# Kernel optimization log

Measured on AMD Instinct MI355X. Metric: run time of the kernel, lower is better.

Reference implementation:

```python
import jax, jax.numpy as jnp
import numpy as np


def setup_inputs() -> dict:
    key = jax.random.key(0)
    k1, k2, k3, k4 = jax.random.split(key, 4)
    B, T, C, H = 4, 2048, 1024, 64
    x = jax.random.normal(k1, (B, T, C), dtype=jnp.float32)
    # nn.Linear(n_embd, head_size, bias=False) weights, stored as [in, out]
    s = 1.0 / np.sqrt(C)
    Wk = jax.random.normal(k2, (C, H), dtype=jnp.float32) * s
    Wq = jax.random.normal(k3, (C, H), dtype=jnp.float32) * s
    Wv = jax.random.normal(k4, (C, H), dtype=jnp.float32) * s
    return {"x": x, "Wk": Wk, "Wq": Wq, "Wv": Wv}


def reference(x, Wk, Wq, Wv):
    B, T, C = x.shape
    k = x @ Wk  # [B,T,H]
    q = x @ Wq  # [B,T,H]
    v = x @ Wv  # [B,T,H]
    # NOTE: original scales by C**-0.5 where C = n_embd (faithful quirk).
    scale = jnp.asarray(C, x.dtype) ** -0.5
    wei = jnp.einsum('bth,bsh->bts', q, k) * scale  # [B,T,T]
    causal = jnp.tril(jnp.ones((T, T), dtype=bool))
    wei = jnp.where(causal, wei, -jnp.inf)
    wei = jax.nn.softmax(wei, axis=-1)
    # dropout is identity in eval mode / for deterministic reference
    return jnp.einsum('bts,bsh->bth', wei, v)
```

## Files before the change

kernel.cpp:

```cpp
#include <hip/hip_runtime.h>

#define B_ 4
#define T_ 2048
#define C_ 1024
#define H_ 64
#define M_ (B_*T_)

typedef __bf16 bf16x8 __attribute__((ext_vector_type(8)));
typedef float f32x4 __attribute__((ext_vector_type(4)));
typedef short short8 __attribute__((ext_vector_type(8)));
typedef short short4v __attribute__((ext_vector_type(4)));
typedef float float4v __attribute__((ext_vector_type(4)));

static __device__ __forceinline__ f32x4 mfma16(bf16x8 a, bf16x8 b, f32x4 c) {
    return __builtin_amdgcn_mfma_f32_16x16x32_bf16(a, b, c, 0, 0, 0);
}
static __device__ __forceinline__ unsigned short f2bfu(float f) {
    return __builtin_bit_cast(unsigned short, (__bf16)f);
}

__global__ __launch_bounds__(256) void wconv_kernel(const float* __restrict__ Wk,
                                                    const float* __restrict__ Wq,
                                                    const float* __restrict__ Wv,
                                                    unsigned short* __restrict__ Wtf) {
    int t = blockIdx.x * 256 + threadIdx.x;
    int f = t >> 6;
    int l = t & 63;
    int n = f % 12, kk = f / 12;
    int sel = n >> 2;
    int wcol = (n & 3) * 16 + (l & 15);
    int kbase = kk * 32 + (l >> 4) * 8;
    const float* W = (sel == 0) ? Wk : ((sel == 1) ? Wq : Wv);
    float scale = (sel == 1) ? 0.03125f : 1.0f;
    unsigned short* dst = Wtf + f * 512 + l * 8;
#pragma unroll
    for (int j = 0; j < 8; ++j)
        dst[j] = f2bfu(W[(kbase + j) * 64 + wcol] * scale);
}

__global__ __launch_bounds__(256) void proj_kernel(const float* __restrict__ x,
                                                   const unsigned short* __restrict__ Wtf,
                                                   unsigned short* __restrict__ kbuf,
                                                   unsigned short* __restrict__ qbuf,
                                                   unsigned short* __restrict__ vbuf) {
    int tid = threadIdx.x;
    int l = tid & 63, lm = l & 15, lg = l >> 4;
    int w = tid >> 6;
    int r0 = blockIdx.x * 16;

    f32x4 acc[3];
#pragma unroll
    for (int nn = 0; nn < 3; ++nn) acc[nn] = f32x4{0.f, 0.f, 0.f, 0.f};

    const float* xp = x + (r0 + lm) * C_ + lg * 8;
    const unsigned short* wp = Wtf + (w * 3) * 512 + l * 8;

    float4v a0 = *(const float4v*)(xp);
    float4v a1 = *(const float4v*)(xp + 4);
    short8 b0 = *(const short8*)(wp);
    short8 b1 = *(const short8*)(wp + 512);
    short8 b2 = *(const short8*)(wp + 1024);

    for (int kk = 0; kk < 31; ++kk) {
        xp += 32; wp += 12 * 512;
        float4v na0 = *(const float4v*)(xp);
        float4v na1 = *(const float4v*)(xp + 4);
        short8 nb0 = *(const short8*)(wp);
        short8 nb1 = *(const short8*)(wp + 512);
        short8 nb2 = *(const short8*)(wp + 1024);
        bf16x8 af;
#pragma unroll
        for (int j = 0; j < 4; ++j) { af[j] = (__bf16)a0[j]; af[4 + j] = (__bf16)a1[j]; }
        acc[0] = mfma16(af, __builtin_bit_cast(bf16x8, b0), acc[0]);
        acc[1] = mfma16(af, __builtin_bit_cast(bf16x8, b1), acc[1]);
        acc[2] = mfma16(af, __builtin_bit_cast(bf16x8, b2), acc[2]);
        a0 = na0; a1 = na1; b0 = nb0; b1 = nb1; b2 = nb2;
    }
    {
        bf16x8 af;
#pragma unroll
        for (int j = 0; j < 4; ++j) { af[j] = (__bf16)a0[j]; af[4 + j] = (__bf16)a1[j]; }
        acc[0] = mfma16(af, __builtin_bit_cast(bf16x8, b0), acc[0]);
        acc[1] = mfma16(af, __builtin_bit_cast(bf16x8, b1), acc[1]);
        acc[2] = mfma16(af, __builtin_bit_cast(bf16x8, b2), acc[2]);
    }

    int tg0 = r0 + lg * 4;
#pragma unroll
    for (int nn = 0; nn < 3; ++nn) {
        int n = w * 3 + nn;
        int sel = n >> 2;
        int col = (n & 3) * 16 + lm;
        unsigned short* dst = (sel == 0) ? kbuf : ((sel == 1) ? qbuf : vbuf);
#pragma unroll
        for (int i = 0; i < 4; ++i)
            dst[(tg0 + i) * H_ + col] = f2bfu(acc[nn][i]);
    }
}

__global__ __launch_bounds__(256) void kvconv_kernel(unsigned short* __restrict__ kbuf,
                                                     unsigned short* __restrict__ vbuf) {
    __shared__ alignas(16) unsigned short klds[32][72];
    __shared__ alignas(16) unsigned short vlds[32][72];
    int tid = threadIdx.x;
    int bj = blockIdx.x;
    unsigned short* kt = kbuf + bj * 2048;
    unsigned short* vt = vbuf + bj * 2048;

    int row = tid >> 3, cq = (tid & 7) * 8;
    short8 kv = *(const short8*)(kt + row * 64 + cq);
    short8 vv = *(const short8*)(vt + row * 64 + cq);
    *(short8*)(&klds[row][cq]) = kv;
    *(short8*)(&vlds[row][cq]) = vv;
    __syncthreads();

    int l = tid & 63, lm = l & 15, lg = l >> 4;
    int f = tid >> 6;
    int kk = f >> 1, nn = f & 1;
    short8 kf = *(const short8*)(&klds[nn * 16 + lm][kk * 32 + lg * 8]);
    short8 vf;
#pragma unroll
    for (int jj = 0; jj < 8; ++jj)
        vf[jj] = (short)vlds[lg * 8 + jj][f * 16 + lm];

    *(short8*)(kt + f * 512 + l * 8) = kf;
    *(short8*)(vt + f * 512 + l * 8) = vf;
}

__global__ __launch_bounds__(512) void attn_kernel(const unsigned short* __restrict__ kbuf,
                                                   const unsigned short* __restrict__ qbuf,
                                                   const unsigned short* __restrict__ vbuf,
                                                   float* __restrict__ out) {
    int tid = threadIdx.x;
    int l = tid & 63, lm = l & 15, lg = l >> 4;
    int w = tid >> 6;
    int bid = blockIdx.x;
    int xcd = bid & 7, ii = bid >> 3;
    int b = xcd >> 1;
    int qtl = ii * 2 + (xcd & 1);
    int q0 = (127 - qtl) * 16;

    __shared__ alignas(16) unsigned short plds[8][16][72];
    __shared__ float olds[8][16][64];
    __shared__ float mlds[8][16];
    __shared__ float llds[8][16];

    bf16x8 qf[2];
#pragma unroll
    for (int kk = 0; kk < 2; ++kk)
        qf[kk] = __builtin_bit_cast(bf16x8,
            *(const short8*)(qbuf + (b * T_ + q0 + lm) * H_ + kk * 32 + lg * 8));

    f32x4 of[4];
#pragma unroll
    for (int nh = 0; nh < 4; ++nh) of[nh] = f32x4{0.f, 0.f, 0.f, 0.f};
    float mrun = -1e30f, lrun = 0.f;

    int nj = q0 / 64 + 1;

    for (int J = w; J < nj; J += 8) {
        f32x4 s[4];
#pragma unroll
        for (int n = 0; n < 4; ++n) s[n] = f32x4{0.f, 0.f, 0.f, 0.f};
#pragma unroll
        for (int kk = 0; kk < 2; ++kk) {
#pragma unroll
            for (int n = 0; n < 4; ++n) {
                const unsigned short* kp = kbuf +
                    (((b * 64 + 2 * J + (n >> 1)) * 2 + kk) * 2 + (n & 1)) * 512 + l * 8;
                s[n] = mfma16(__builtin_bit_cast(bf16x8, *(const short8*)kp), qf[kk], s[n]);
            }
        }
        if (J == nj - 1) {
            int qr = q0 + lm;
#pragma unroll
            for (int n = 0; n < 4; ++n) {
                int kc0 = J * 64 + (n >> 1) * 32 + (n & 1) * 16 + lg * 4;
#pragma unroll
                for (int i = 0; i < 4; ++i)
                    if (kc0 + i > qr) s[n][i] = -1e30f;
            }
        }
        float pm0 = fmaxf(fmaxf(s[0][0], s[0][1]), fmaxf(s[0][2], s[0][3]));
        float pm1 = fmaxf(fmaxf(s[1][0], s[1][1]), fmaxf(s[1][2], s[1][3]));
        float pm2 = fmaxf(fmaxf(s[2][0], s[2][1]), fmaxf(s[2][2], s[2][3]));
        float pm3 = fmaxf(fmaxf(s[3][0], s[3][1]), fmaxf(s[3][2], s[3][3]));
        float pm = fmaxf(fmaxf(pm0, pm1), fmaxf(pm2, pm3));
        pm = fmaxf(pm, __shfl_xor(pm, 16, 64));
        pm = fmaxf(pm, __shfl_xor(pm, 32, 64));
        float mn = fmaxf(mrun, pm);
        float al = __expf(mrun - mn);
        float rsn[4];
#pragma unroll
        for (int n = 0; n < 4; ++n) {
            float e0 = __expf(s[n][0] - mn), e1 = __expf(s[n][1] - mn);
            float e2 = __expf(s[n][2] - mn), e3 = __expf(s[n][3] - mn);
            s[n][0] = e0; s[n][1] = e1; s[n][2] = e2; s[n][3] = e3;
            rsn[n] = (e0 + e1) + (e2 + e3);
        }
        float rs = (rsn[0] + rsn[1]) + (rsn[2] + rsn[3]);
        rs += __shfl_xor(rs, 16, 64);
        rs += __shfl_xor(rs, 32, 64);
        lrun = lrun * al + rs;
        mrun = mn;
        float alv[4];
#pragma unroll
        for (int i = 0; i < 4; ++i) alv[i] = __shfl(al, lg * 4 + i, 64);
#pragma unroll
        for (int nh = 0; nh < 4; ++nh)
#pragma unroll
            for (int i = 0; i < 4; ++i) of[nh][i] *= alv[i];

#pragma unroll
        for (int n = 0; n < 4; ++n) {
            short4v pv;
#pragma unroll
            for (int i = 0; i < 4; ++i) pv[i] = (short)f2bfu(s[n][i]);
            *(short4v*)(&plds[w][lm][(n >> 1) * 32 + (n & 1) * 16 + lg * 4]) = pv;
        }
        bf16x8 pf[2];
#pragma unroll
        for (int ks = 0; ks < 2; ++ks)
            pf[ks] = __builtin_bit_cast(bf16x8,
                *(const short8*)(&plds[w][lm][ks * 32 + lg * 8]));
#pragma unroll
        for (int nh = 0; nh < 4; ++nh) {
#pragma unroll
            for (int ks = 0; ks < 2; ++ks) {
                const unsigned short* vp = vbuf +
                    ((b * 64 + 2 * J + ks) * 4 + nh) * 512 + l * 8;
                of[nh] = mfma16(pf[ks], __builtin_bit_cast(bf16x8, *(const short8*)vp), of[nh]);
            }
        }
    }

#pragma unroll
    for (int nh = 0; nh < 4; ++nh)
#pragma unroll
        for (int i = 0; i < 4; ++i)
            olds[w][lg * 4 + i][nh * 16 + lm] = of[nh][i];
    if (l < 16) {
        mlds[w][l] = mrun;
        llds[w][l] = lrun;
    }
    __syncthreads();

    int row = tid >> 5;
    int c0 = tid & 31;
    float mw[8];
#pragma unroll
    for (int u = 0; u < 8; ++u) mw[u] = mlds[u][row];
    float M = fmaxf(fmaxf(fmaxf(mw[0], mw[1]), fmaxf(mw[2], mw[3])),
                    fmaxf(fmaxf(mw[4], mw[5]), fmaxf(mw[6], mw[7])));
    float ew[8];
    float L = 0.f;
#pragma unroll
    for (int u = 0; u < 8; ++u) { ew[u] = __expf(mw[u] - M); L += llds[u][row] * ew[u]; }
    float invL = 1.0f / L;
#pragma unroll
    for (int h = 0; h < 2; ++h) {
        int col = c0 + h * 32;
        float o = 0.f;
#pragma unroll
        for (int u = 0; u < 8; ++u) o += olds[u][row][col] * ew[u];
        out[(b * T_ + q0 + row) * H_ + col] = o * invL;
    }
}

extern "C" void kernel_launch(void* const* d_in, const int* in_sizes, int n_in,
                              void* d_out, int out_size, void* d_ws, size_t ws_size,
                              hipStream_t stream) {
    const float* x  = (const float*)d_in[0];
    const float* Wk = (const float*)d_in[1];
    const float* Wq = (const float*)d_in[2];
    const float* Wv = (const float*)d_in[3];
    float* out = (float*)d_out;

    unsigned short* ws   = (unsigned short*)d_ws;
    unsigned short* Wtf  = ws;
    unsigned short* kbuf = Wtf + 384 * 512;
    unsigned short* qbuf = kbuf + M_ * H_;
    unsigned short* vbuf = qbuf + M_ * H_;

    wconv_kernel<<<dim3(96), dim3(256), 0, stream>>>(Wk, Wq, Wv, Wtf);
    proj_kernel<<<dim3(M_ / 16), dim3(256), 0, stream>>>(x, Wtf, kbuf, qbuf, vbuf);
    kvconv_kernel<<<dim3(B_ * 64), dim3(256), 0, stream>>>(kbuf, vbuf);
    attn_kernel<<<dim3(B_ * (T_ / 16)), dim3(512), 0, stream>>>(kbuf, qbuf, vbuf, out);
}
```

Baseline: 106.9 us.

## Merge all stages into one cooperative persistent kernel with grid syncs

```diff
diff --git a/kernel.cpp b/kernel.cpp
--- a/kernel.cpp
+++ b/kernel.cpp
@@ -1,4 +1,5 @@
 #include <hip/hip_runtime.h>
+#include <hip/hip_cooperative_groups.h>
 
 #define B_ 4
 #define T_ 2048
@@ -19,251 +20,254 @@
     return __builtin_bit_cast(unsigned short, (__bf16)f);
 }
 
-__global__ __launch_bounds__(256) void wconv_kernel(const float* __restrict__ Wk,
-                                                    const float* __restrict__ Wq,
-                                                    const float* __restrict__ Wv,
-                                                    unsigned short* __restrict__ Wtf) {
-    int t = blockIdx.x * 256 + threadIdx.x;
-    int f = t >> 6;
-    int l = t & 63;
-    int n = f % 12, kk = f / 12;
-    int sel = n >> 2;
-    int wcol = (n & 3) * 16 + (l & 15);
-    int kbase = kk * 32 + (l >> 4) * 8;
-    const float* W = (sel == 0) ? Wk : ((sel == 1) ? Wq : Wv);
-    float scale = (sel == 1) ? 0.03125f : 1.0f;
-    unsigned short* dst = Wtf + f * 512 + l * 8;
-#pragma unroll
-    for (int j = 0; j < 8; ++j)
-        dst[j] = f2bfu(W[(kbase + j) * 64 + wcol] * scale);
-}
-
-__global__ __launch_bounds__(256) void proj_kernel(const float* __restrict__ x,
-                                                   const unsigned short* __restrict__ Wtf,
-                                                   unsigned short* __restrict__ kbuf,
-                                                   unsigned short* __restrict__ qbuf,
-                                                   unsigned short* __restrict__ vbuf) {
+struct SmemAttn {
+    unsigned short plds[8][16][72];
+    float olds[8][16][64];
+    float mlds[8][16];
+    float llds[8][16];
+};
+struct SmemProj {
+    float red[2][12][64][4];
+    unsigned short stage[3][16][72];
+};
+union alignas(16) Smem { SmemAttn a; SmemProj p; };
+
+__global__ __launch_bounds__(512, 4) void mega_kernel(
+        const float* __restrict__ x,
+        const float* __restrict__ Wk, const float* __restrict__ Wq,
+        const float* __restrict__ Wv,
+        unsigned short* __restrict__ ws, float* __restrict__ out, int mode) {
+    __shared__ Smem sm;
+    unsigned short* Wtf  = ws;
+    unsigned short* kbuf = ws + 196608;
+    unsigned short* qfb  = kbuf + 524288;
+    unsigned short* vbuf = qfb + 524288;
+
     int tid = threadIdx.x;
+    int bid = blockIdx.x;
     int l = tid & 63, lm = l & 15, lg = l >> 4;
     int w = tid >> 6;
-    int r0 = blockIdx.x * 16;
-
-    f32x4 acc[3];
-#pragma unroll
-    for (int nn = 0; nn < 3; ++nn) acc[nn] = f32x4{0.f, 0.f, 0.f, 0.f};
-
-    const float* xp = x + (r0 + lm) * C_ + lg * 8;
-    const unsigned short* wp = Wtf + (w * 3) * 512 + l * 8;
-
-    float4v a0 = *(const float4v*)(xp);
-    float4v a1 = *(const float4v*)(xp + 4);
-    short8 b0 = *(const short8*)(wp);
-    short8 b1 = *(const short8*)(wp + 512);
-    short8 b2 = *(const short8*)(wp + 1024);
-
-    for (int kk = 0; kk < 31; ++kk) {
-        xp += 32; wp += 12 * 512;
-        float4v na0 = *(const float4v*)(xp);
-        float4v na1 = *(const float4v*)(xp + 4);
-        short8 nb0 = *(const short8*)(wp);
-        short8 nb1 = *(const short8*)(wp + 512);
-        short8 nb2 = *(const short8*)(wp + 1024);
-        bf16x8 af;
-#pragma unroll
-        for (int j = 0; j < 4; ++j) { af[j] = (__bf16)a0[j]; af[4 + j] = (__bf16)a1[j]; }
-        acc[0] = mfma16(af, __builtin_bit_cast(bf16x8, b0), acc[0]);
-        acc[1] = mfma16(af, __builtin_bit_cast(bf16x8, b1), acc[1]);
-        acc[2] = mfma16(af, __builtin_bit_cast(bf16x8, b2), acc[2]);
-        a0 = na0; a1 = na1; b0 = nb0; b1 = nb1; b2 = nb2;
-    }
+
+    if ((mode == 3 || mode == 0) && bid < 48) {
+        int t = bid * 512 + tid;
+        int f = t >> 6, la = t & 63;
+        int n = f % 12, kk = f / 12;
+        int sel = n >> 2;
+        int wcol = (n & 3) * 16 + (la & 15);
+        int kbase = kk * 32 + (la >> 4) * 8;
+        const float* W = (sel == 0) ? Wk : ((sel == 1) ? Wq : Wv);
+        float scale = (sel == 1) ? 0.03125f : 1.0f;
+        unsigned short* dst = Wtf + f * 512 + la * 8;
+#pragma unroll
+        for (int j = 0; j < 8; ++j)
+            dst[j] = f2bfu(W[(kbase + j) * 64 + wcol] * scale);
+    }
+    if (mode == 3) cooperative_groups::this_grid().sync();
+
+    if (mode == 3 || mode == 1) {
+        int r0 = bid * 16;
+        int khalf = w >> 2;
+        int c3 = (w & 3) * 3;
+        f32x4 acc[3];
+#pragma unroll
+        for (int nn = 0; nn < 3; ++nn) acc[nn] = f32x4{0.f, 0.f, 0.f, 0.f};
+
+        const float* xp = x + (r0 + lm) * C_ + khalf * 512 + lg * 8;
+        const unsigned short* wp = Wtf + (khalf * 16 * 12 + c3) * 512 + l * 8;
+
+        float4v a0 = *(const float4v*)(xp);
+        float4v a1 = *(const float4v*)(xp + 4);
+        short8 b0 = *(const short8*)(wp);
+        short8 b1 = *(const short8*)(wp + 512);
+        short8 b2 = *(const short8*)(wp + 1024);
+        for (int kk = 0; kk < 15; ++kk) {
+            xp += 32; wp += 12 * 512;
+            float4v na0 = *(const float4v*)(xp);
+            float4v na1 = *(const float4v*)(xp + 4);
+            short8 nb0 = *(const short8*)(wp);
+            short8 nb1 = *(const short8*)(wp + 512);
+            short8 nb2 = *(const short8*)(wp + 1024);
+            bf16x8 af;
+#pragma unroll
+            for (int j = 0; j < 4; ++j) { af[j] = (__bf16)a0[j]; af[4 + j] = (__bf16)a1[j]; }
+            acc[0] = mfma16(af, __builtin_bit_cast(bf16x8, b0), acc[0]);
+            acc[1] = mfma16(af, __builtin_bit_cast(bf16x8, b1), acc[1]);
+            acc[2] = mfma16(af, __builtin_bit_cast(bf16x8, b2), acc[2]);
+            a0 = na0; a1 = na1; b0 = nb0; b1 = nb1; b2 = nb2;
+        }
+        {
+            bf16x8 af;
+#pragma unroll
+            for (int j = 0; j < 4; ++j) { af[j] = (__bf16)a0[j]; af[4 + j] = (__bf16)a1[j]; }
+            acc[0] = mfma16(af, __builtin_bit_cast(bf16x8, b0), acc[0]);
+            acc[1] = mfma16(af, __builtin_bit_cast(bf16x8, b1), acc[1]);
+            acc[2] = mfma16(af, __builtin_bit_cast(bf16x8, b2), acc[2]);
+        }
+#pragma unroll
+        for (int nn = 0; nn < 3; ++nn)
+            *(f32x4*)&sm.p.red[khalf][c3 + nn][l][0] = acc[nn];
+        __syncthreads();
+
+        for (int idx = tid; idx < 768; idx += 512) {
+            int tile = idx >> 6, l2 = idx & 63, lm2 = l2 & 15, lg2 = l2 >> 4;
+            f32x4 s0 = *(const f32x4*)&sm.p.red[0][tile][l2][0];
+            f32x4 s1 = *(const f32x4*)&sm.p.red[1][tile][l2][0];
+            int sel = tile >> 2, colb = (tile & 3) * 16 + lm2;
+#pragma unroll
+            for (int i = 0; i < 4; ++i)
+                sm.p.stage[sel][lg2 * 4 + i][colb] = f2bfu(s0[i] + s1[i]);
+        }
+        __syncthreads();
+
+        int bq = bid >> 7;
+        int jt = (bid & 127) >> 1;
+        int nn = bid & 1;
+        int base = (bq * 64 + jt) * 2048;
+        if (w < 2) {
+            short8 v = *(const short8*)&sm.p.stage[0][lm][w * 32 + lg * 8];
+            *(short8*)(kbuf + base + w * 1024 + nn * 512 + l * 8) = v;
+        } else if (w < 4) {
+            int kkq = w - 2;
+            short8 v = *(const short8*)&sm.p.stage[1][lm][kkq * 32 + lg * 8];
+            *(short8*)(qfb + bid * 1024 + kkq * 512 + l * 8) = v;
+        } else if (l < 32) {
+            int nh = w - 4;
+            short8 v;
+#pragma unroll
+            for (int j = 0; j < 8; ++j)
+                v[j] = (short)sm.p.stage[2][(l >> 4) * 8 + j][nh * 16 + (l & 15)];
+            *(short8*)(vbuf + base + nh * 512 + nn * 256 + l * 8) = v;
+        }
+    }
+    if (mode == 3) cooperative_groups::this_grid().sync();
+
+    if (!(mode == 3 || mode == 2)) return;
     {
-        bf16x8 af;
-#pragma unroll
-        for (int j = 0; j < 4; ++j) { af[j] = (__bf16)a0[j]; af[4 + j] = (__bf16)a1[j]; }
-        acc[0] = mfma16(af, __builtin_bit_cast(bf16x8, b0), acc[0]);
-        acc[1] = mfma16(af, __builtin_bit_cast(bf16x8, b1), acc[1]);
-        acc[2] = mfma16(af, __builtin_bit_cast(bf16x8, b2), acc[2]);
-    }
-
-    int tg0 = r0 + lg * 4;
-#pragma unroll
-    for (int nn = 0; nn < 3; ++nn) {
-        int n = w * 3 + nn;
-        int sel = n >> 2;
-        int col = (n & 3) * 16 + lm;
-        unsigned short* dst = (sel == 0) ? kbuf : ((sel == 1) ? qbuf : vbuf);
-#pragma unroll
-        for (int i = 0; i < 4; ++i)
-            dst[(tg0 + i) * H_ + col] = f2bfu(acc[nn][i]);
-    }
-}
-
-__global__ __launch_bounds__(256) void kvconv_kernel(unsigned short* __restrict__ kbuf,
-                                                     unsigned short* __restrict__ vbuf) {
-    __shared__ alignas(16) unsigned short klds[32][72];
-    __shared__ alignas(16) unsigned short vlds[32][72];
-    int tid = threadIdx.x;
-    int bj = blockIdx.x;
-    unsigned short* kt = kbuf + bj * 2048;
-    unsigned short* vt = vbuf + bj * 2048;
-
-    int row = tid >> 3, cq = (tid & 7) * 8;
-    short8 kv = *(const short8*)(kt + row * 64 + cq);
-    short8 vv = *(const short8*)(vt + row * 64 + cq);
-    *(short8*)(&klds[row][cq]) = kv;
-    *(short8*)(&vlds[row][cq]) = vv;
-    __syncthreads();
-
-    int l = tid & 63, lm = l & 15, lg = l >> 4;
-    int f = tid >> 6;
-    int kk = f >> 1, nn = f & 1;
-    short8 kf = *(const short8*)(&klds[nn * 16 + lm][kk * 32 + lg * 8]);
-    short8 vf;
-#pragma unroll
-    for (int jj = 0; jj < 8; ++jj)
-        vf[jj] = (short)vlds[lg * 8 + jj][f * 16 + lm];
-
-    *(short8*)(kt + f * 512 + l * 8) = kf;
-    *(short8*)(vt + f * 512 + l * 8) = vf;
-}
-
-__global__ __launch_bounds__(512) void attn_kernel(const unsigned short* __restrict__ kbuf,
-                                                   const unsigned short* __restrict__ qbuf,
-                                                   const unsigned short* __restrict__ vbuf,
-                                                   float* __restrict__ out) {
-    int tid = threadIdx.x;
-    int l = tid & 63, lm = l & 15, lg = l >> 4;
-    int w = tid >> 6;
-    int bid = blockIdx.x;
-    int xcd = bid & 7, ii = bid >> 3;
-    int b = xcd >> 1;
-    int qtl = ii * 2 + (xcd & 1);
-    int q0 = (127 - qtl) * 16;
-
-    __shared__ alignas(16) unsigned short plds[8][16][72];
-    __shared__ float olds[8][16][64];
-    __shared__ float mlds[8][16];
-    __shared__ float llds[8][16];
-
-    bf16x8 qf[2];
-#pragma unroll
-    for (int kk = 0; kk < 2; ++kk)
-        qf[kk] = __builtin_bit_cast(bf16x8,
-            *(const short8*)(qbuf + (b * T_ + q0 + lm) * H_ + kk * 32 + lg * 8));
-
-    f32x4 of[4];
-#pragma unroll
-    for (int nh = 0; nh < 4; ++nh) of[nh] = f32x4{0.f, 0.f, 0.f, 0.f};
-    float mrun = -1e30f, lrun = 0.f;
-
-    int nj = q0 / 64 + 1;
-
-    for (int J = w; J < nj; J += 8) {
-        f32x4 s[4];
-#pragma unroll
-        for (int n = 0; n < 4; ++n) s[n] = f32x4{0.f, 0.f, 0.f, 0.f};
-#pragma unroll
-        for (int kk = 0; kk < 2; ++kk) {
+        int xcd = bid & 7, ii = bid >> 3;
+        int b = xcd >> 1;
+        int qtl = ii * 2 + (xcd & 1);
+        int q0 = (127 - qtl) * 16;
+
+        bf16x8 qf[2];
+#pragma unroll
+        for (int kk = 0; kk < 2; ++kk)
+            qf[kk] = __builtin_bit_cast(bf16x8,
+                *(const short8*)(qfb + (b * 128 + (q0 >> 4)) * 1024 + kk * 512 + l * 8));
+
+        f32x4 of[4];
+#pragma unroll
+        for (int nh = 0; nh < 4; ++nh) of[nh] = f32x4{0.f, 0.f, 0.f, 0.f};
+        float mrun = -1e30f, lrun = 0.f;
+
+        int nj = q0 / 64 + 1;
+
+        for (int J = w; J < nj; J += 8) {
+            f32x4 s[4];
+#pragma unroll
+            for (int n = 0; n < 4; ++n) s[n] = f32x4{0.f, 0.f, 0.f, 0.f};
+#pragma unroll
+            for (int kk = 0; kk < 2; ++kk) {
+#pragma unroll
+                for (int n = 0; n < 4; ++n) {
+                    const unsigned short* kp = kbuf +
+                        (((b * 64 + 2 * J + (n >> 1)) * 2 + kk) * 2 + (n & 1)) * 512 + l * 8;
+                    s[n] = mfma16(__builtin_bit_cast(bf16x8, *(const short8*)kp), qf[kk], s[n]);
+                }
+            }
+            if (J == nj - 1) {
+                int qr = q0 + lm;
+#pragma unroll
+                for (int n = 0; n < 4; ++n) {
+                    int kc0 = J * 64 + (n >> 1) * 32 + (n & 1) * 16 + lg * 4;
+#pragma unroll
+                    for (int i = 0; i < 4; ++i)
+                        if (kc0 + i > qr) s[n][i] = -1e30f;
+                }
+            }
+            float pm0 = fmaxf(fmaxf(s[0][0], s[0][1]), fmaxf(s[0][2], s[0][3]));
+            float pm1 = fmaxf(fmaxf(s[1][0], s[1][1]), fmaxf(s[1][2], s[1][3]));
+            float pm2 = fmaxf(fmaxf(s[2][0], s[2][1]), fmaxf(s[2][2], s[2][3]));
+            float pm3 = fmaxf(fmaxf(s[3][0], s[3][1]), fmaxf(s[3][2], s[3][3]));
+            float pm = fmaxf(fmaxf(pm0, pm1), fmaxf(pm2, pm3));
+            pm = fmaxf(pm, __shfl_xor(pm, 16, 64));
+            pm = fmaxf(pm, __shfl_xor(pm, 32, 64));
+            float mn = fmaxf(mrun, pm);
+            float al = __expf(mrun - mn);
+            float rsn[4];
 #pragma unroll
             for (int n = 0; n < 4; ++n) {
-                const unsigned short* kp = kbuf +
-                    (((b * 64 + 2 * J + (n >> 1)) * 2 + kk) * 2 + (n & 1)) * 512 + l * 8;
-                s[n] = mfma16(__builtin_bit_cast(bf16x8, *(const short8*)kp), qf[kk], s[n]);
-            }
-        }
-        if (J == nj - 1) {
-            int qr = q0 + lm;
+                float e0 = __expf(s[n][0] - mn), e1 = __expf(s[n][1] - mn);
+                float e2 = __expf(s[n][2] - mn), e3 = __expf(s[n][3] - mn);
+                s[n][0] = e0; s[n][1] = e1; s[n][2] = e2; s[n][3] = e3;
+                rsn[n] = (e0 + e1) + (e2 + e3);
+            }
+            float rs = (rsn[0] + rsn[1]) + (rsn[2] + rsn[3]);
+            rs += __shfl_xor(rs, 16, 64);
+            rs += __shfl_xor(rs, 32, 64);
+            lrun = lrun * al + rs;
+            mrun = mn;
+            float alv[4];
+#pragma unroll
+            for (int i = 0; i < 4; ++i) alv[i] = __shfl(al, lg * 4 + i, 64);
+#pragma unroll
+            for (int nh = 0; nh < 4; ++nh)
+#pragma unroll
+                for (int i = 0; i < 4; ++i) of[nh][i] *= alv[i];
+
 #pragma unroll
             for (int n = 0; n < 4; ++n) {
-                int kc0 = J * 64 + (n >> 1) * 32 + (n & 1) * 16 + lg * 4;
-#pragma unroll
-                for (int i = 0; i < 4; ++i)
-                    if (kc0 + i > qr) s[n][i] = -1e30f;
-            }
-        }
-        float pm0 = fmaxf(fmaxf(s[0][0], s[0][1]), fmaxf(s[0][2], s[0][3]));
-        float pm1 = fmaxf(fmaxf(s[1][0], s[1][1]), fmaxf(s[1][2], s[1][3]));
-        float pm2 = fmaxf(fmaxf(s[2][0], s[2][1]), fmaxf(s[2][2], s[2][3]));
-        float pm3 = fmaxf(fmaxf(s[3][0], s[3][1]), fmaxf(s[3][2], s[3][3]));
-        float pm = fmaxf(fmaxf(pm0, pm1), fmaxf(pm2, pm3));
-        pm = fmaxf(pm, __shfl_xor(pm, 16, 64));
-        pm = fmaxf(pm, __shfl_xor(pm, 32, 64));
-        float mn = fmaxf(mrun, pm);
-        float al = __expf(mrun - mn);
-        float rsn[4];
-#pragma unroll
-        for (int n = 0; n < 4; ++n) {
-            float e0 = __expf(s[n][0] - mn), e1 = __expf(s[n][1] - mn);
-            float e2 = __expf(s[n][2] - mn), e3 = __expf(s[n][3] - mn);
-            s[n][0] = e0; s[n][1] = e1; s[n][2] = e2; s[n][3] = e3;
-            rsn[n] = (e0 + e1) + (e2 + e3);
-        }
-        float rs = (rsn[0] + rsn[1]) + (rsn[2] + rsn[3]);
-        rs += __shfl_xor(rs, 16, 64);
-        rs += __shfl_xor(rs, 32, 64);
-        lrun = lrun * al + rs;
-        mrun = mn;
-        float alv[4];
-#pragma unroll
-        for (int i = 0; i < 4; ++i) alv[i] = __shfl(al, lg * 4 + i, 64);
+                short4v pv;
+#pragma unroll
+                for (int i = 0; i < 4; ++i) pv[i] = (short)f2bfu(s[n][i]);
+                *(short4v*)(&sm.a.plds[w][lm][(n >> 1) * 32 + (n & 1) * 16 + lg * 4]) = pv;
+            }
+            bf16x8 pf[2];
+#pragma unroll
+            for (int ks = 0; ks < 2; ++ks)
+                pf[ks] = __builtin_bit_cast(bf16x8,
+                    *(const short8*)(&sm.a.plds[w][lm][ks * 32 + lg * 8]));
+#pragma unroll
+            for (int nh = 0; nh < 4; ++nh) {
+#pragma unroll
+                for (int ks = 0; ks < 2; ++ks) {
+                    const unsigned short* vp = vbuf +
+                        ((b * 64 + 2 * J + ks) * 4 + nh) * 512 + l * 8;
+                    of[nh] = mfma16(pf[ks], __builtin_bit_cast(bf16x8, *(const short8*)vp), of[nh]);
+                }
+            }
+        }
+
 #pragma unroll
         for (int nh = 0; nh < 4; ++nh)
 #pragma unroll
-            for (int i = 0; i < 4; ++i) of[nh][i] *= alv[i];
-
-#pragma unroll
-        for (int n = 0; n < 4; ++n) {
-            short4v pv;
-#pragma unroll
-            for (int i = 0; i < 4; ++i) pv[i] = (short)f2bfu(s[n][i]);
-            *(short4v*)(&plds[w][lm][(n >> 1) * 32 + (n & 1) * 16 + lg * 4]) = pv;
-        }
-        bf16x8 pf[2];
-#pragma unroll
-        for (int ks = 0; ks < 2; ++ks)
-            pf[ks] = __builtin_bit_cast(bf16x8,
-                *(const short8*)(&plds[w][lm][ks * 32 + lg * 8]));
-#pragma unroll
-        for (int nh = 0; nh < 4; ++nh) {
-#pragma unroll
-            for (int ks = 0; ks < 2; ++ks) {
-                const unsigned short* vp = vbuf +
-                    ((b * 64 + 2 * J + ks) * 4 + nh) * 512 + l * 8;
-                of[nh] = mfma16(pf[ks], __builtin_bit_cast(bf16x8, *(const short8*)vp), of[nh]);
-            }
-        }
-    }
-
-#pragma unroll
-    for (int nh = 0; nh < 4; ++nh)
-#pragma unroll
-        for (int i = 0; i < 4; ++i)
-            olds[w][lg * 4 + i][nh * 16 + lm] = of[nh][i];
-    if (l < 16) {
-        mlds[w][l] = mrun;
-        llds[w][l] = lrun;
-    }
-    __syncthreads();
-
-    int row = tid >> 5;
-    int c0 = tid & 31;
-    float mw[8];
-#pragma unroll
-    for (int u = 0; u < 8; ++u) mw[u] = mlds[u][row];
-    float M = fmaxf(fmaxf(fmaxf(mw[0], mw[1]), fmaxf(mw[2], mw[3])),
-                    fmaxf(fmaxf(mw[4], mw[5]), fmaxf(mw[6], mw[7])));
-    float ew[8];
-    float L = 0.f;
-#pragma unroll
-    for (int u = 0; u < 8; ++u) { ew[u] = __expf(mw[u] - M); L += llds[u][row] * ew[u]; }
-    float invL = 1.0f / L;
-#pragma unroll
-    for (int h = 0; h < 2; ++h) {
-        int col = c0 + h * 32;
-        float o = 0.f;
-#pragma unroll
-        for (int u = 0; u < 8; ++u) o += olds[u][row][col] * ew[u];
-        out[(b * T_ + q0 + row) * H_ + col] = o * invL;
+            for (int i = 0; i < 4; ++i)
+                sm.a.olds[w][lg * 4 + i][nh * 16 + lm] = of[nh][i];
+        if (l < 16) {
+            sm.a.mlds[w][l] = mrun;
+            sm.a.llds[w][l] = lrun;
+        }
+        __syncthreads();
+
+        int row = tid >> 5;
+        int c0 = tid & 31;
+        float mw[8];
+#pragma unroll
+        for (int u = 0; u < 8; ++u) mw[u] = sm.a.mlds[u][row];
+        float M = fmaxf(fmaxf(fmaxf(mw[0], mw[1]), fmaxf(mw[2], mw[3])),
+                        fmaxf(fmaxf(mw[4], mw[5]), fmaxf(mw[6], mw[7])));
+        float ew[8];
+        float L = 0.f;
+#pragma unroll
+        for (int u = 0; u < 8; ++u) { ew[u] = __expf(mw[u] - M); L += sm.a.llds[u][row] * ew[u]; }
+        float invL = 1.0f / L;
+#pragma unroll
+        for (int h = 0; h < 2; ++h) {
+            int col = c0 + h * 32;
+            float o = 0.f;
+#pragma unroll
+            for (int u = 0; u < 8; ++u) o += sm.a.olds[u][row][col] * ew[u];
+            out[(b * T_ + q0 + row) * H_ + col] = o * invL;
+        }
     }
 }
 
@@ -274,16 +278,17 @@
     const float* Wk = (const float*)d_in[1];
     const float* Wq = (const float*)d_in[2];
     const float* Wv = (const float*)d_in[3];
-    float* out = (float*)d_out;
-
-    unsigned short* ws   = (unsigned short*)d_ws;
-    unsigned short* Wtf  = ws;
-    unsigned short* kbuf = Wtf + 384 * 512;
-    unsigned short* qbuf = kbuf + M_ * H_;
-    unsigned short* vbuf = qbuf + M_ * H_;
-
-    wconv_kernel<<<dim3(96), dim3(256), 0, stream>>>(Wk, Wq, Wv, Wtf);
-    proj_kernel<<<dim3(M_ / 16), dim3(256), 0, stream>>>(x, Wtf, kbuf, qbuf, vbuf);
-    kvconv_kernel<<<dim3(B_ * 64), dim3(256), 0, stream>>>(kbuf, vbuf);
-    attn_kernel<<<dim3(B_ * (T_ / 16)), dim3(512), 0, stream>>>(kbuf, qbuf, vbuf, out);
-}
+    unsigned short* ws = (unsigned short*)d_ws;
+    float* o = (float*)d_out;
+
+    int mode = 3;
+    void* args[] = {(void*)&x, (void*)&Wk, (void*)&Wq, (void*)&Wv,
+                    (void*)&ws, (void*)&o, (void*)&mode};
+    hipError_t rc = hipLaunchCooperativeKernel(
+        reinterpret_cast<void*>(mega_kernel), dim3(512), dim3(512), args, 0, stream);
+    if (rc != hipSuccess) {
+        mega_kernel<<<dim3(512), dim3(512), 0, stream>>>(x, Wk, Wq, Wv, ws, o, 0);
+        mega_kernel<<<dim3(512), dim3(512), 0, stream>>>(x, Wk, Wq, Wv, ws, o, 1);
+        mega_kernel<<<dim3(512), dim3(512), 0, stream>>>(x, Wk, Wq, Wv, ws, o, 2);
+    }
+}
```

After: 235.1 us. 2.2x slower.
